# Optimization experiments

Hardware: AMD Instinct MI355X
Metric: run time of the kernel (lower is better)

The kernel has to match this reference:

```python
import jax, jax.numpy as jnp
import numpy as np

B, NPG, DEG = 8, 4096, 8          # graphs, nodes/graph, avg degree
N, E = B * NPG, B * NPG * DEG      # total nodes / directed edges
IN_C, HID, NCLS = 1024, 512, 4
K1, K2 = NPG // 2, NPG // 4        # ceil(0.5*NPG), ceil(0.5*K1)
NEG = 1e30                         # large-negative for masked scores


def setup_inputs() -> dict:
    key = jax.random.key(0)
    ks = jax.random.split(key, 20)
    gid = jnp.arange(E, dtype=jnp.int32) // (NPG * DEG)  # graph id per edge
    edge_src = jax.random.randint(ks[0], (E,), 0, NPG, dtype=jnp.int32) + gid * NPG
    edge_dst = jax.random.randint(ks[1], (E,), 0, NPG, dtype=jnp.int32) + gid * NPG
    x = jax.random.normal(ks[2], (N, IN_C), jnp.float32)

    def w(k, shape):
        fan_in = shape[0]
        return jax.random.normal(k, shape, jnp.float32) * (1.0 / np.sqrt(fan_in))

    return dict(
        x=x, edge_src=edge_src, edge_dst=edge_dst,
        W1=w(ks[3], (IN_C, HID)), b1=jnp.zeros((HID,), jnp.float32),
        p1_wr=w(ks[4], (HID, 1)), p1_br=jnp.zeros((1,), jnp.float32), p1_wo=w(ks[5], (HID, 1)),
        W2=w(ks[6], (HID, HID)), b2=jnp.zeros((HID,), jnp.float32),
        p2_wr=w(ks[7], (HID, 1)), p2_br=jnp.zeros((1,), jnp.float32), p2_wo=w(ks[8], (HID, 1)),
        W3=w(ks[9], (HID, HID)), b3=jnp.zeros((HID,), jnp.float32),
        fc1_w=w(ks[10], (2 * HID, HID)), fc1_b=jnp.zeros((HID,), jnp.float32),
        fc2_w=w(ks[11], (HID, NCLS)), fc2_b=jnp.zeros((NCLS,), jnp.float32),
    )


def _gcn(x, src, dst, emask, nmask, W, b):
    # PyG GCNConv: add self-loops, sym-normalize, aggregate, bias.
    h = x @ W                                             # [N,H]
    deg = jax.ops.segment_sum(emask, dst, num_segments=N) + nmask  # self-loop for active nodes
    dinv = jnp.where(deg > 0, jax.lax.rsqrt(deg), 0.0)
    coef = dinv[src] * dinv[dst] * emask                  # [E]
    out = jax.ops.segment_sum(h[src] * coef[:, None], dst, num_segments=N)
    out = out + (dinv * dinv * nmask)[:, None] * h + b    # self-loop term + bias
    return out


def _sag_pool(x, src, dst, emask, nmask, wr, br, wo, k):
    # PyG SAGPooling(GraphConv score, ratio): keep per-graph top-k, x *= tanh(score).
    agg = jax.ops.segment_sum(x[src] * emask[:, None], dst, num_segments=N)
    score = (agg @ wr + br + x @ wo)[:, 0]                # GraphConv(HID->1)
    score = jnp.where(nmask > 0, score, -NEG)
    order = jnp.argsort(-score.reshape(B, NPG), axis=1)
    ranks = jnp.argsort(order, axis=1)                    # rank within graph, descending score
    keep = (ranks < k).reshape(-1).astype(x.dtype) * nmask
    x2 = x * jnp.tanh(score)[:, None] * keep[:, None]
    emask2 = emask * keep[src] * keep[dst]                # filter edges to kept nodes
    return x2, emask2, keep


def reference(x, edge_src, edge_dst,
              W1, b1, p1_wr, p1_br, p1_wo,
              W2, b2, p2_wr, p2_br, p2_wo,
              W3, b3, fc1_w, fc1_b, fc2_w, fc2_b):
    src, dst = edge_src, edge_dst
    lrelu = lambda t: jax.nn.leaky_relu(t, 0.01)
    nmask = jnp.ones((N,), x.dtype)
    emask = jnp.ones((E,), x.dtype)

    h = lrelu(_gcn(x, src, dst, emask, nmask, W1, b1))
    h, emask, nmask = _sag_pool(h, src, dst, emask, nmask, p1_wr, p1_br, p1_wo, K1)
    h = lrelu(_gcn(h, src, dst, emask, nmask, W2, b2))
    h, emask, nmask = _sag_pool(h, src, dst, emask, nmask, p2_wr, p2_br, p2_wo, K2)
    h = lrelu(_gcn(h, src, dst, emask, nmask, W3, b3))

    hb = h.reshape(B, NPG, HID)
    mb = nmask.reshape(B, NPG)
    x_mean = (hb * mb[..., None]).sum(1) / mb.sum(1)[:, None]   # global_mean_pool over kept nodes
    x_max = jnp.where(mb[..., None] > 0, hb, -jnp.inf).max(1)   # global_max_pool
    g = jnp.concatenate([x_mean, x_max], axis=1)                # [B, 2H]; dropout is eval-mode identity
    g = lrelu(g @ fc1_w + fc1_b)
    return g @ fc2_w + fc2_b                                    # [B, NCLS]
```

## Files before the change

### kernel.cpp

```cpp
#include <hip/hip_runtime.h>

#define N_NODES 32768
#define NPG_    4096
#define NB_     8
#define E_EDGES 262144
#define IN_C_   1024
#define HID_    512
#define NOUT_   512
#define K1_     2048
#define K2_     1024

typedef _Float16 half4_t __attribute__((ext_vector_type(4)));
typedef _Float16 half8_t __attribute__((ext_vector_type(8)));
typedef float    floatx4 __attribute__((ext_vector_type(4)));

__device__ __forceinline__ float lrelu(float v) { return v > 0.f ? v : 0.01f * v; }

template <bool AFP32>
__global__ __launch_bounds__(256) void gemm_split_kernel(
    const float* __restrict__ A32,
    const _Float16* __restrict__ Ah, const _Float16* __restrict__ Al,
    const _Float16* __restrict__ Bh, const _Float16* __restrict__ Bl,
    float* __restrict__ C, int K) {
  __shared__ __align__(16) _Float16 sAh[128][64];
  __shared__ __align__(16) _Float16 sAl[128][64];
  __shared__ __align__(16) _Float16 sBh[128][64];
  __shared__ __align__(16) _Float16 sBl[128][64];

  const int t    = threadIdx.x;
  const int bm   = blockIdx.y * 128;
  const int bn   = blockIdx.x * 128;
  const int lane = t & 63;
  const int wv   = t >> 6;
  const int wr   = wv >> 1;
  const int wc   = wv & 1;
  const int fr   = lane & 15;
  const int kg   = lane >> 4;

  floatx4 zero = {0.f, 0.f, 0.f, 0.f};
  floatx4 acc[4][4];
#pragma unroll
  for (int i = 0; i < 4; ++i)
#pragma unroll
    for (int j = 0; j < 4; ++j) acc[i][j] = zero;

  for (int kt = 0; kt < K; kt += 64) {
#pragma unroll
    for (int l = 0; l < 4; ++l) {
      const int idx = l * 256 + t;
      const int row = idx >> 3;
      const int slot = idx & 7;
      const int col = ((slot ^ (row & 7)) << 3);
      *(half8_t*)&sBh[row][col] = *(const half8_t*)(Bh + (size_t)(bn + row) * K + kt + slot * 8);
      *(half8_t*)&sBl[row][col] = *(const half8_t*)(Bl + (size_t)(bn + row) * K + kt + slot * 8);
    }
    if constexpr (AFP32) {
#pragma unroll
      for (int l = 0; l < 8; ++l) {
        const int idx = l * 256 + t;
        const int row = idx >> 4;
        const int c4  = idx & 15;
        const float4 v = *(const float4*)(A32 + (size_t)(bm + row) * K + kt + c4 * 4);
        const _Float16 h0 = (_Float16)v.x, h1 = (_Float16)v.y,
                       h2 = (_Float16)v.z, h3 = (_Float16)v.w;
        half4_t hh = {h0, h1, h2, h3};
        half4_t hl = {(_Float16)(v.x - (float)h0), (_Float16)(v.y - (float)h1),
                      (_Float16)(v.z - (float)h2), (_Float16)(v.w - (float)h3)};
        const int slot = c4 >> 1;
        const int col  = ((slot ^ (row & 7)) << 3) + (c4 & 1) * 4;
        *(half4_t*)&sAh[row][col] = hh;
        *(half4_t*)&sAl[row][col] = hl;
      }
    } else {
#pragma unroll
      for (int l = 0; l < 4; ++l) {
        const int idx = l * 256 + t;
        const int row = idx >> 3;
        const int slot = idx & 7;
        const int col = ((slot ^ (row & 7)) << 3);
        *(half8_t*)&sAh[row][col] = *(const half8_t*)(Ah + (size_t)(bm + row) * K + kt + slot * 8);
        *(half8_t*)&sAl[row][col] = *(const half8_t*)(Al + (size_t)(bm + row) * K + kt + slot * 8);
      }
    }
    __syncthreads();

#pragma unroll
    for (int ks = 0; ks < 2; ++ks) {
      half8_t ahf[4], alf[4], bhf[4], blf[4];
      const int slot = ks * 4 + kg;
#pragma unroll
      for (int i = 0; i < 4; ++i) {
        const int row = wr * 64 + i * 16 + fr;
        const int col = ((slot ^ (row & 7)) << 3);
        ahf[i] = *(const half8_t*)&sAh[row][col];
        alf[i] = *(const half8_t*)&sAl[row][col];
      }
#pragma unroll
      for (int j = 0; j < 4; ++j) {
        const int nrow = wc * 64 + j * 16 + fr;
        const int col  = ((slot ^ (nrow & 7)) << 3);
        bhf[j] = *(const half8_t*)&sBh[nrow][col];
        blf[j] = *(const half8_t*)&sBl[nrow][col];
      }
#pragma unroll
      for (int i = 0; i < 4; ++i)
#pragma unroll
        for (int j = 0; j < 4; ++j) {
          acc[i][j] = __builtin_amdgcn_mfma_f32_16x16x32_f16(ahf[i], bhf[j], acc[i][j], 0, 0, 0);
          acc[i][j] = __builtin_amdgcn_mfma_f32_16x16x32_f16(ahf[i], blf[j], acc[i][j], 0, 0, 0);
          acc[i][j] = __builtin_amdgcn_mfma_f32_16x16x32_f16(alf[i], bhf[j], acc[i][j], 0, 0, 0);
        }
    }
    __syncthreads();
  }

#pragma unroll
  for (int i = 0; i < 4; ++i)
#pragma unroll
    for (int j = 0; j < 4; ++j) {
      const int row0 = bm + wr * 64 + i * 16 + kg * 4;
      const int col  = bn + wc * 64 + j * 16 + fr;
#pragma unroll
      for (int r = 0; r < 4; ++r)
        C[(size_t)(row0 + r) * NOUT_ + col] = acc[i][j][r];
    }
}

__global__ void split_w_kernel(const float* __restrict__ W, int K, int total,
                               _Float16* __restrict__ Wht, _Float16* __restrict__ Wlt) {
  const int idx = blockIdx.x * blockDim.x + threadIdx.x;
  if (idx >= total) return;
  const int n = idx / K;
  const int k = idx - n * K;
  const float v = W[(size_t)k * NOUT_ + n];
  const _Float16 h = (_Float16)v;
  Wht[idx] = h;
  Wlt[idx] = (_Float16)(v - (float)h);
}

__global__ void csr_count_kernel(const int* __restrict__ dst, int* __restrict__ cnt) {
  const int e = blockIdx.x * blockDim.x + threadIdx.x;
  if (e < E_EDGES) atomicAdd(&cnt[dst[e]], 1);
}

__global__ __launch_bounds__(1024) void exscan_kernel(const int* __restrict__ cnt,
                                                      int* __restrict__ ofs,
                                                      int* __restrict__ cur) {
  __shared__ int part[1024];
  const int t = threadIdx.x;
  const int base = t * 32;
  int loc[32];
  int s = 0;
#pragma unroll
  for (int i = 0; i < 32; ++i) { loc[i] = cnt[base + i]; s += loc[i]; }
  part[t] = s;
  __syncthreads();
  for (int off = 1; off < 1024; off <<= 1) {
    const int v = (t >= off) ? part[t - off] : 0;
    __syncthreads();
    part[t] += v;
    __syncthreads();
  }
  int run = (t > 0) ? part[t - 1] : 0;
#pragma unroll
  for (int i = 0; i < 32; ++i) { ofs[base + i] = run; cur[base + i] = run; run += loc[i]; }
  if (t == 1023) ofs[N_NODES] = run;
}

__global__ void csr_fill_kernel(const int* __restrict__ src, const int* __restrict__ dst,
                                int* __restrict__ cur, int* __restrict__ csr_src) {
  const int e = blockIdx.x * blockDim.x + threadIdx.x;
  if (e < E_EDGES) {
    const int p = atomicAdd(&cur[dst[e]], 1);
    csr_src[p] = src[e];
  }
}

__global__ void dinv_kernel(const int* __restrict__ ofs, const int* __restrict__ csr,
                            const float* __restrict__ m, float* __restrict__ dinv) {
  const int n = blockIdx.x * blockDim.x + threadIdx.x;
  if (n >= N_NODES) return;
  const float mn = m[n];
  float d = mn;
  if (mn > 0.f) {
    const int s = ofs[n], e = ofs[n + 1];
    for (int i = s; i < e; ++i) d += m[csr[i]];
  }
  dinv[n] = d > 0.f ? 1.f / sqrtf(d) : 0.f;
}

__global__ __launch_bounds__(128) void gcn_agg_kernel(const float* __restrict__ h,
                                                      const int* __restrict__ ofs,
                                                      const int* __restrict__ csr,
                                                      const float* __restrict__ dinv,
                                                      const float* __restrict__ bias,
                                                      float* __restrict__ out) {
  const int n = blockIdx.x;
  const int t = threadIdx.x;
  const float dn = dinv[n];
  float4 acc = {0.f, 0.f, 0.f, 0.f};
  if (dn > 0.f) {
    const int s = ofs[n], e = ofs[n + 1];
    for (int i = s; i < e; ++i) {
      const int sv = csr[i];
      const float c = dinv[sv] * dn;
      if (c != 0.f) {
        const float4 hv = *(const float4*)(h + (size_t)sv * HID_ + t * 4);
        acc.x += c * hv.x; acc.y += c * hv.y; acc.z += c * hv.z; acc.w += c * hv.w;
      }
    }
  }
  const float4 hv = *(const float4*)(h + (size_t)n * HID_ + t * 4);
  const float4 bv = *(const float4*)(bias + t * 4);
  const float sc = dn * dn;
  float4 r;
  r.x = lrelu(acc.x + sc * hv.x + bv.x);
  r.y = lrelu(acc.y + sc * hv.y + bv.y);
  r.z = lrelu(acc.z + sc * hv.z + bv.z);
  r.w = lrelu(acc.w + sc * hv.w + bv.w);
  *(float4*)(out + (size_t)n * HID_ + t * 4) = r;
}

__global__ __launch_bounds__(64) void node_dots_kernel(const float* __restrict__ h,
                                                       const float* __restrict__ wr,
                                                       const float* __restrict__ wo,
                                                       float* __restrict__ sr,
                                                       float* __restrict__ so) {
  const int n = blockIdx.x;
  const int t = threadIdx.x;
  const float4 h0 = *(const float4*)(h + (size_t)n * HID_ + t * 8);
  const float4 h1 = *(const float4*)(h + (size_t)n * HID_ + t * 8 + 4);
  const float4 r0 = *(const float4*)(wr + t * 8);
  const float4 r1 = *(const float4*)(wr + t * 8 + 4);
  const float4 o0 = *(const float4*)(wo + t * 8);
  const float4 o1 = *(const float4*)(wo + t * 8 + 4);
  float pr = h0.x * r0.x + h0.y * r0.y + h0.z * r0.z + h0.w * r0.w +
             h1.x * r1.x + h1.y * r1.y + h1.z * r1.z + h1.w * r1.w;
  float po = h0.x * o0.x + h0.y * o0.y + h0.z * o0.z + h0.w * o0.w +
             h1.x * o1.x + h1.y * o1.y + h1.z * o1.z + h1.w * o1.w;
#pragma unroll
  for (int off = 32; off; off >>= 1) {
    pr += __shfl_down(pr, off);
    po += __shfl_down(po, off);
  }
  if (t == 0) { sr[n] = pr; so[n] = po; }
}

__global__ void score_kernel(const int* __restrict__ ofs, const int* __restrict__ csr,
                             const float* __restrict__ sr, const float* __restrict__ so,
                             const float* __restrict__ m, const float* __restrict__ br,
                             float* __restrict__ score) {
  const int n = blockIdx.x * blockDim.x + threadIdx.x;
  if (n >= N_NODES) return;
  if (m[n] <= 0.f) { score[n] = -1e30f; return; }
  float s = 0.f;
  const int st = ofs[n], e = ofs[n + 1];
  for (int i = st; i < e; ++i) { const int sv = csr[i]; s += sr[sv] * m[sv]; }
  score[n] = s + so[n] + br[0];
}

__global__ __launch_bounds__(256) void topk_kernel(const float* __restrict__ score,
                                                   const float* __restrict__ m,
                                                   float* __restrict__ mout, int k) {
  __shared__ float ssc[NPG_];
  const int g   = blockIdx.x >> 4;
  const int blk = blockIdx.x & 15;
  const float* gs = score + g * NPG_;
  for (int i = threadIdx.x; i < NPG_; i += 256) ssc[i] = gs[i];
  __syncthreads();
  const int li = blk * 256 + threadIdx.x;
  const float mysc = ssc[li];
  int cnt = 0;
#pragma unroll 4
  for (int j = 0; j < NPG_; ++j) {
    const float sj = ssc[j];
    cnt += (sj > mysc) || (sj == mysc && j < li);
  }
  const int n = g * NPG_ + li;
  mout[n] = (cnt < k && m[n] > 0.f) ? 1.f : 0.f;
}

__global__ void pool_apply_split_kernel(const float* __restrict__ xin,
                                        const float* __restrict__ score,
                                        const float* __restrict__ keep,
                                        _Float16* __restrict__ Ph,
                                        _Float16* __restrict__ Pl) {
  const int i = blockIdx.x * blockDim.x + threadIdx.x;
  const int n = i >> 7;
  const float f = keep[n] > 0.f ? tanhf(score[n]) : 0.f;
  const float4 v = *(const float4*)(xin + (size_t)i * 4);
  const float x0 = v.x * f, x1 = v.y * f, x2 = v.z * f, x3 = v.w * f;
  const _Float16 h0 = (_Float16)x0, h1 = (_Float16)x1,
                 h2 = (_Float16)x2, h3 = (_Float16)x3;
  half4_t hh = {h0, h1, h2, h3};
  half4_t hl = {(_Float16)(x0 - (float)h0), (_Float16)(x1 - (float)h1),
                (_Float16)(x2 - (float)h2), (_Float16)(x3 - (float)h3)};
  *(half4_t*)(Ph + (size_t)i * 4) = hh;
  *(half4_t*)(Pl + (size_t)i * 4) = hl;
}

__global__ __launch_bounds__(512) void gpool1_kernel(const float* __restrict__ h,
                                                     const float* __restrict__ m,
                                                     float* __restrict__ psum,
                                                     float* __restrict__ pmax,
                                                     float* __restrict__ pcnt) {
  const int b = blockIdx.y;
  const int c = blockIdx.x;
  const int ch = threadIdx.x;
  const int base = b * NPG_ + c * 128;
  float s = 0.f, mx = -INFINITY, cv = 0.f;
  for (int i = 0; i < 128; ++i) {
    const float mv = m[base + i];
    const float hv = h[(size_t)(base + i) * HID_ + ch];
    s += mv * hv;
    if (mv > 0.f) mx = fmaxf(mx, hv);
    cv += mv;
  }
  const int p = b * 32 + c;
  psum[(size_t)p * HID_ + ch] = s;
  pmax[(size_t)p * HID_ + ch] = mx;
  if (ch == 0) pcnt[p] = cv;
}

__global__ __launch_bounds__(512) void gpool2_kernel(const float* __restrict__ psum,
                                                     const float* __restrict__ pmax,
                                                     const float* __restrict__ pcnt,
                                                     float* __restrict__ g) {
  const int b = blockIdx.x;
  const int ch = threadIdx.x;
  float s = 0.f, mx = -INFINITY, cv = 0.f;
  for (int c = 0; c < 32; ++c) {
    const int p = b * 32 + c;
    s += psum[(size_t)p * HID_ + ch];
    mx = fmaxf(mx, pmax[(size_t)p * HID_ + ch]);
    cv += pcnt[p];
  }
  g[b * 1024 + ch] = s / cv;
  g[b * 1024 + 512 + ch] = mx;
}

__global__ __launch_bounds__(64) void fc1_kernel(const float* __restrict__ g,
                                                 const float* __restrict__ w1,
                                                 const float* __restrict__ b1,
                                                 float* __restrict__ hbuf) {
  const int b = blockIdx.x;
  const int j = blockIdx.y * 64 + threadIdx.x;
  __shared__ float gs[2 * HID_];
  for (int i = threadIdx.x; i < 2 * HID_; i += 64) gs[i] = g[b * 1024 + i];
  __syncthreads();
  float s = b1[j];
#pragma unroll 4
  for (int i = 0; i < 2 * HID_; ++i) s += gs[i] * w1[i * HID_ + j];
  hbuf[b * HID_ + j] = lrelu(s);
}

__global__ __launch_bounds__(64) void fc2_kernel(const float* __restrict__ hbuf,
                                                 const float* __restrict__ w2,
                                                 const float* __restrict__ b2,
                                                 float* __restrict__ out) {
  const int b = blockIdx.x;
  const int t = threadIdx.x;
  float s0 = 0.f, s1 = 0.f, s2 = 0.f, s3 = 0.f;
  for (int i = t; i < HID_; i += 64) {
    const float hv = hbuf[b * HID_ + i];
    s0 += hv * w2[i * 4 + 0];
    s1 += hv * w2[i * 4 + 1];
    s2 += hv * w2[i * 4 + 2];
    s3 += hv * w2[i * 4 + 3];
  }
#pragma unroll
  for (int off = 32; off; off >>= 1) {
    s0 += __shfl_down(s0, off); s1 += __shfl_down(s1, off);
    s2 += __shfl_down(s2, off); s3 += __shfl_down(s3, off);
  }
  if (t == 0) {
    out[b * 4 + 0] = s0 + b2[0];
    out[b * 4 + 1] = s1 + b2[1];
    out[b * 4 + 2] = s2 + b2[2];
    out[b * 4 + 3] = s3 + b2[3];
  }
}

__global__ void set_ones_kernel(float* __restrict__ p, int n) {
  const int i = blockIdx.x * blockDim.x + threadIdx.x;
  if (i < n) p[i] = 1.f;
}

extern "C" void kernel_launch(void* const* d_in, const int* in_sizes, int n_in,
                              void* d_out, int out_size, void* d_ws, size_t ws_size,
                              hipStream_t stream) {
  const float* x        = (const float*)d_in[0];
  const int*   edge_src = (const int*)d_in[1];
  const int*   edge_dst = (const int*)d_in[2];
  const float* W1 = (const float*)d_in[3];
  const float* b1 = (const float*)d_in[4];
  const float* p1_wr = (const float*)d_in[5];
  const float* p1_br = (const float*)d_in[6];
  const float* p1_wo = (const float*)d_in[7];
  const float* W2 = (const float*)d_in[8];
  const float* b2 = (const float*)d_in[9];
  const float* p2_wr = (const float*)d_in[10];
  const float* p2_br = (const float*)d_in[11];
  const float* p2_wo = (const float*)d_in[12];
  const float* W3 = (const float*)d_in[13];
  const float* b3 = (const float*)d_in[14];
  const float* fc1_w = (const float*)d_in[15];
  const float* fc1_b = (const float*)d_in[16];
  const float* fc2_w = (const float*)d_in[17];
  const float* fc2_b = (const float*)d_in[18];
  float* out = (float*)d_out;

  size_t o = 0;
  auto alloc = [&](size_t bytes) {
    void* p = (char*)d_ws + o;
    o += (bytes + 255) & ~(size_t)255;
    return p;
  };
  float* R0 = (float*)alloc((size_t)N_NODES * HID_ * 4);
  float* R1 = (float*)alloc((size_t)N_NODES * HID_ * 4);
  _Float16* W1ht = (_Float16*)alloc((size_t)NOUT_ * IN_C_ * 2);
  _Float16* W1lt = (_Float16*)alloc((size_t)NOUT_ * IN_C_ * 2);
  _Float16* W2ht = (_Float16*)alloc((size_t)NOUT_ * HID_ * 2);
  _Float16* W2lt = (_Float16*)alloc((size_t)NOUT_ * HID_ * 2);
  _Float16* W3ht = (_Float16*)alloc((size_t)NOUT_ * HID_ * 2);
  _Float16* W3lt = (_Float16*)alloc((size_t)NOUT_ * HID_ * 2);
  int*   csr   = (int*)alloc((size_t)E_EDGES * 4);
  int*   ofs   = (int*)alloc((size_t)(N_NODES + 1) * 4);
  int*   cur   = (int*)alloc((size_t)N_NODES * 4);
  int*   cnt   = (int*)alloc((size_t)N_NODES * 4);
  float* dinvB = (float*)alloc((size_t)N_NODES * 4);
  float* mA    = (float*)alloc((size_t)N_NODES * 4);
  float* mB    = (float*)alloc((size_t)N_NODES * 4);
  float* srB   = (float*)alloc((size_t)N_NODES * 4);
  float* soB   = (float*)alloc((size_t)N_NODES * 4);
  float* scB   = (float*)alloc((size_t)N_NODES * 4);
  float* psum  = (float*)alloc((size_t)NB_ * 32 * HID_ * 4);
  float* pmax  = (float*)alloc((size_t)NB_ * 32 * HID_ * 4);
  float* pcnt  = (float*)alloc((size_t)NB_ * 32 * 4);
  float* gbuf  = (float*)alloc((size_t)NB_ * 1024 * 4);
  float* hbuf  = (float*)alloc((size_t)NB_ * HID_ * 4);

  _Float16* P1h = (_Float16*)R0;
  _Float16* P1l = P1h + (size_t)N_NODES * HID_;
  _Float16* P2h = (_Float16*)R1;
  _Float16* P2l = P2h + (size_t)N_NODES * HID_;

  hipMemsetAsync(cnt, 0, (size_t)N_NODES * 4, stream);
  csr_count_kernel<<<E_EDGES / 256, 256, 0, stream>>>(edge_dst, cnt);
  exscan_kernel<<<1, 1024, 0, stream>>>(cnt, ofs, cur);
  csr_fill_kernel<<<E_EDGES / 256, 256, 0, stream>>>(edge_src, edge_dst, cur, csr);
  set_ones_kernel<<<N_NODES / 256, 256, 0, stream>>>(mA, N_NODES);
  split_w_kernel<<<(NOUT_ * IN_C_) / 256, 256, 0, stream>>>(W1, IN_C_, NOUT_ * IN_C_, W1ht, W1lt);
  split_w_kernel<<<(NOUT_ * HID_) / 256, 256, 0, stream>>>(W2, HID_, NOUT_ * HID_, W2ht, W2lt);
  split_w_kernel<<<(NOUT_ * HID_) / 256, 256, 0, stream>>>(W3, HID_, NOUT_ * HID_, W3ht, W3lt);

  const dim3 gemm_grid(NOUT_ / 128, N_NODES / 128);

  gemm_split_kernel<true><<<gemm_grid, 256, 0, stream>>>(x, nullptr, nullptr,
                                                         W1ht, W1lt, R0, IN_C_);
  dinv_kernel<<<N_NODES / 256, 256, 0, stream>>>(ofs, csr, mA, dinvB);
  gcn_agg_kernel<<<N_NODES, 128, 0, stream>>>(R0, ofs, csr, dinvB, b1, R1);
  node_dots_kernel<<<N_NODES, 64, 0, stream>>>(R1, p1_wr, p1_wo, srB, soB);
  score_kernel<<<N_NODES / 256, 256, 0, stream>>>(ofs, csr, srB, soB, mA, p1_br, scB);
  topk_kernel<<<NB_ * 16, 256, 0, stream>>>(scB, mA, mB, K1_);
  pool_apply_split_kernel<<<(N_NODES * HID_ / 4) / 256, 256, 0, stream>>>(R1, scB, mB, P1h, P1l);

  gemm_split_kernel<false><<<gemm_grid, 256, 0, stream>>>(nullptr, P1h, P1l,
                                                          W2ht, W2lt, R1, HID_);
  dinv_kernel<<<N_NODES / 256, 256, 0, stream>>>(ofs, csr, mB, dinvB);
  gcn_agg_kernel<<<N_NODES, 128, 0, stream>>>(R1, ofs, csr, dinvB, b2, R0);
  node_dots_kernel<<<N_NODES, 64, 0, stream>>>(R0, p2_wr, p2_wo, srB, soB);
  score_kernel<<<N_NODES / 256, 256, 0, stream>>>(ofs, csr, srB, soB, mB, p2_br, scB);
  topk_kernel<<<NB_ * 16, 256, 0, stream>>>(scB, mB, mA, K2_);
  pool_apply_split_kernel<<<(N_NODES * HID_ / 4) / 256, 256, 0, stream>>>(R0, scB, mA, P2h, P2l);

  gemm_split_kernel<false><<<gemm_grid, 256, 0, stream>>>(nullptr, P2h, P2l,
                                                          W3ht, W3lt, R0, HID_);
  dinv_kernel<<<N_NODES / 256, 256, 0, stream>>>(ofs, csr, mA, dinvB);
  gcn_agg_kernel<<<N_NODES, 128, 0, stream>>>(R0, ofs, csr, dinvB, b3, R1);

  gpool1_kernel<<<dim3(32, NB_), 512, 0, stream>>>(R1, mA, psum, pmax, pcnt);
  gpool2_kernel<<<NB_, 512, 0, stream>>>(psum, pmax, pcnt, gbuf);
  fc1_kernel<<<dim3(NB_, HID_ / 64), 64, 0, stream>>>(gbuf, fc1_w, fc1_b, hbuf);
  fc2_kernel<<<NB_, 64, 0, stream>>>(hbuf, fc2_w, fc2_b, out);
}
```

Baseline: 1.009 ms.

## Fold source dinv scaling into GEMM epilogue and fuse score dots into aggregation

```diff
diff --git a/kernel.cpp b/kernel.cpp
--- a/kernel.cpp
+++ b/kernel.cpp
@@ -21,6 +21,7 @@
     const float* __restrict__ A32,
     const _Float16* __restrict__ Ah, const _Float16* __restrict__ Al,
     const _Float16* __restrict__ Bh, const _Float16* __restrict__ Bl,
+    const float* __restrict__ dinv,
     float* __restrict__ C, int K) {
   __shared__ __align__(16) _Float16 sAh[128][64];
   __shared__ __align__(16) _Float16 sAl[128][64];
@@ -28,8 +29,11 @@
   __shared__ __align__(16) _Float16 sBl[128][64];
 
   const int t    = threadIdx.x;
-  const int bm   = blockIdx.y * 128;
-  const int bn   = blockIdx.x * 128;
+  const int nwg  = gridDim.x;
+  const int per  = nwg >> 3;
+  const int id   = (blockIdx.x & 7) * per + (blockIdx.x >> 3);
+  const int bn   = (id & 3) * 128;
+  const int bm   = (id >> 2) * 128;
   const int lane = t & 63;
   const int wv   = t >> 6;
   const int wr   = wv >> 1;
@@ -115,15 +119,19 @@
   }
 
 #pragma unroll
-  for (int i = 0; i < 4; ++i)
+  for (int i = 0; i < 4; ++i) {
+    const int row0 = bm + wr * 64 + i * 16 + kg * 4;
+    float ds[4];
+#pragma unroll
+    for (int r = 0; r < 4; ++r) ds[r] = dinv[row0 + r];
 #pragma unroll
     for (int j = 0; j < 4; ++j) {
-      const int row0 = bm + wr * 64 + i * 16 + kg * 4;
-      const int col  = bn + wc * 64 + j * 16 + fr;
+      const int col = bn + wc * 64 + j * 16 + fr;
 #pragma unroll
       for (int r = 0; r < 4; ++r)
-        C[(size_t)(row0 + r) * NOUT_ + col] = acc[i][j][r];
-    }
+        C[(size_t)(row0 + r) * NOUT_ + col] = acc[i][j][r] * ds[r];
+    }
+  }
 }
 
 __global__ void split_w_kernel(const float* __restrict__ W, int K, int total,
@@ -189,61 +197,67 @@
   dinv[n] = d > 0.f ? 1.f / sqrtf(d) : 0.f;
 }
 
-__global__ __launch_bounds__(128) void gcn_agg_kernel(const float* __restrict__ h,
-                                                      const int* __restrict__ ofs,
-                                                      const int* __restrict__ csr,
-                                                      const float* __restrict__ dinv,
-                                                      const float* __restrict__ bias,
-                                                      float* __restrict__ out) {
-  const int n = blockIdx.x;
-  const int t = threadIdx.x;
+template <bool DOTS>
+__global__ __launch_bounds__(256) void gcn_agg_fused_kernel(
+    const float* __restrict__ hs,
+    const int* __restrict__ ofs, const int* __restrict__ csr,
+    const float* __restrict__ dinv, const float* __restrict__ bias,
+    const float* __restrict__ wr, const float* __restrict__ wo,
+    float* __restrict__ out, float* __restrict__ sr, float* __restrict__ so) {
+  const int n = blockIdx.x * 4 + (threadIdx.x >> 6);
+  const int t = threadIdx.x & 63;
+  const size_t c0 = (size_t)t * 8;
   const float dn = dinv[n];
-  float4 acc = {0.f, 0.f, 0.f, 0.f};
+  floatx4 a0 = {0.f, 0.f, 0.f, 0.f}, a1 = a0, b0 = a0, b1 = a0;
   if (dn > 0.f) {
     const int s = ofs[n], e = ofs[n + 1];
-    for (int i = s; i < e; ++i) {
-      const int sv = csr[i];
-      const float c = dinv[sv] * dn;
-      if (c != 0.f) {
-        const float4 hv = *(const float4*)(h + (size_t)sv * HID_ + t * 4);
-        acc.x += c * hv.x; acc.y += c * hv.y; acc.z += c * hv.z; acc.w += c * hv.w;
-      }
-    }
-  }
-  const float4 hv = *(const float4*)(h + (size_t)n * HID_ + t * 4);
-  const float4 bv = *(const float4*)(bias + t * 4);
-  const float sc = dn * dn;
-  float4 r;
-  r.x = lrelu(acc.x + sc * hv.x + bv.x);
-  r.y = lrelu(acc.y + sc * hv.y + bv.y);
-  r.z = lrelu(acc.z + sc * hv.z + bv.z);
-  r.w = lrelu(acc.w + sc * hv.w + bv.w);
-  *(float4*)(out + (size_t)n * HID_ + t * 4) = r;
-}
-
-__global__ __launch_bounds__(64) void node_dots_kernel(const float* __restrict__ h,
-                                                       const float* __restrict__ wr,
-                                                       const float* __restrict__ wo,
-                                                       float* __restrict__ sr,
-                                                       float* __restrict__ so) {
-  const int n = blockIdx.x;
-  const int t = threadIdx.x;
-  const float4 h0 = *(const float4*)(h + (size_t)n * HID_ + t * 8);
-  const float4 h1 = *(const float4*)(h + (size_t)n * HID_ + t * 8 + 4);
-  const float4 r0 = *(const float4*)(wr + t * 8);
-  const float4 r1 = *(const float4*)(wr + t * 8 + 4);
-  const float4 o0 = *(const float4*)(wo + t * 8);
-  const float4 o1 = *(const float4*)(wo + t * 8 + 4);
-  float pr = h0.x * r0.x + h0.y * r0.y + h0.z * r0.z + h0.w * r0.w +
-             h1.x * r1.x + h1.y * r1.y + h1.z * r1.z + h1.w * r1.w;
-  float po = h0.x * o0.x + h0.y * o0.y + h0.z * o0.z + h0.w * o0.w +
-             h1.x * o1.x + h1.y * o1.y + h1.z * o1.z + h1.w * o1.w;
-#pragma unroll
-  for (int off = 32; off; off >>= 1) {
-    pr += __shfl_down(pr, off);
-    po += __shfl_down(po, off);
-  }
-  if (t == 0) { sr[n] = pr; so[n] = po; }
+    int i = s;
+    for (; i + 2 <= e; i += 2) {
+      const int s0 = csr[i], s1 = csr[i + 1];
+      const floatx4 v00 = *(const floatx4*)(hs + (size_t)s0 * HID_ + c0);
+      const floatx4 v01 = *(const floatx4*)(hs + (size_t)s0 * HID_ + c0 + 4);
+      const floatx4 v10 = *(const floatx4*)(hs + (size_t)s1 * HID_ + c0);
+      const floatx4 v11 = *(const floatx4*)(hs + (size_t)s1 * HID_ + c0 + 4);
+      a0 += v00; a1 += v01; b0 += v10; b1 += v11;
+    }
+    if (i < e) {
+      const int s0 = csr[i];
+      a0 += *(const floatx4*)(hs + (size_t)s0 * HID_ + c0);
+      a1 += *(const floatx4*)(hs + (size_t)s0 * HID_ + c0 + 4);
+    }
+    a0 += *(const floatx4*)(hs + (size_t)n * HID_ + c0);
+    a1 += *(const floatx4*)(hs + (size_t)n * HID_ + c0 + 4);
+    a0 += b0; a1 += b1;
+  }
+  const floatx4 bv0 = *(const floatx4*)(bias + c0);
+  const floatx4 bv1 = *(const floatx4*)(bias + c0 + 4);
+  floatx4 r0, r1;
+#pragma unroll
+  for (int q = 0; q < 4; ++q) {
+    r0[q] = lrelu(dn * a0[q] + bv0[q]);
+    r1[q] = lrelu(dn * a1[q] + bv1[q]);
+  }
+  *(floatx4*)(out + (size_t)n * HID_ + c0)     = r0;
+  *(floatx4*)(out + (size_t)n * HID_ + c0 + 4) = r1;
+
+  if constexpr (DOTS) {
+    const floatx4 wr0 = *(const floatx4*)(wr + c0);
+    const floatx4 wr1 = *(const floatx4*)(wr + c0 + 4);
+    const floatx4 wo0 = *(const floatx4*)(wo + c0);
+    const floatx4 wo1 = *(const floatx4*)(wo + c0 + 4);
+    float pr = 0.f, po = 0.f;
+#pragma unroll
+    for (int q = 0; q < 4; ++q) {
+      pr += r0[q] * wr0[q] + r1[q] * wr1[q];
+      po += r0[q] * wo0[q] + r1[q] * wo1[q];
+    }
+#pragma unroll
+    for (int off = 32; off; off >>= 1) {
+      pr += __shfl_down(pr, off);
+      po += __shfl_down(po, off);
+    }
+    if (t == 0) { sr[n] = pr; so[n] = po; }
+  }
 }
 
 __global__ void score_kernel(const int* __restrict__ ofs, const int* __restrict__ csr,
@@ -454,30 +468,32 @@
   split_w_kernel<<<(NOUT_ * HID_) / 256, 256, 0, stream>>>(W2, HID_, NOUT_ * HID_, W2ht, W2lt);
   split_w_kernel<<<(NOUT_ * HID_) / 256, 256, 0, stream>>>(W3, HID_, NOUT_ * HID_, W3ht, W3lt);
 
-  const dim3 gemm_grid(NOUT_ / 128, N_NODES / 128);
-
+  const int gemm_grid = (NOUT_ / 128) * (N_NODES / 128);
+  const int agg_grid = N_NODES / 4;
+
+  dinv_kernel<<<N_NODES / 256, 256, 0, stream>>>(ofs, csr, mA, dinvB);
   gemm_split_kernel<true><<<gemm_grid, 256, 0, stream>>>(x, nullptr, nullptr,
-                                                         W1ht, W1lt, R0, IN_C_);
-  dinv_kernel<<<N_NODES / 256, 256, 0, stream>>>(ofs, csr, mA, dinvB);
-  gcn_agg_kernel<<<N_NODES, 128, 0, stream>>>(R0, ofs, csr, dinvB, b1, R1);
-  node_dots_kernel<<<N_NODES, 64, 0, stream>>>(R1, p1_wr, p1_wo, srB, soB);
+                                                         W1ht, W1lt, dinvB, R0, IN_C_);
+  gcn_agg_fused_kernel<true><<<agg_grid, 256, 0, stream>>>(R0, ofs, csr, dinvB, b1,
+                                                           p1_wr, p1_wo, R1, srB, soB);
   score_kernel<<<N_NODES / 256, 256, 0, stream>>>(ofs, csr, srB, soB, mA, p1_br, scB);
   topk_kernel<<<NB_ * 16, 256, 0, stream>>>(scB, mA, mB, K1_);
   pool_apply_split_kernel<<<(N_NODES * HID_ / 4) / 256, 256, 0, stream>>>(R1, scB, mB, P1h, P1l);
 
+  dinv_kernel<<<N_NODES / 256, 256, 0, stream>>>(ofs, csr, mB, dinvB);
   gemm_split_kernel<false><<<gemm_grid, 256, 0, stream>>>(nullptr, P1h, P1l,
-                                                          W2ht, W2lt, R1, HID_);
-  dinv_kernel<<<N_NODES / 256, 256, 0, stream>>>(ofs, csr, mB, dinvB);
-  gcn_agg_kernel<<<N_NODES, 128, 0, stream>>>(R1, ofs, csr, dinvB, b2, R0);
-  node_dots_kernel<<<N_NODES, 64, 0, stream>>>(R0, p2_wr, p2_wo, srB, soB);
+                                                          W2ht, W2lt, dinvB, R1, HID_);
+  gcn_agg_fused_kernel<true><<<agg_grid, 256, 0, stream>>>(R1, ofs, csr, dinvB, b2,
+                                                           p2_wr, p2_wo, R0, srB, soB);
   score_kernel<<<N_NODES / 256, 256, 0, stream>>>(ofs, csr, srB, soB, mB, p2_br, scB);
   topk_kernel<<<NB_ * 16, 256, 0, stream>>>(scB, mB, mA, K2_);
   pool_apply_split_kernel<<<(N_NODES * HID_ / 4) / 256, 256, 0, stream>>>(R0, scB, mA, P2h, P2l);
 
+  dinv_kernel<<<N_NODES / 256, 256, 0, stream>>>(ofs, csr, mA, dinvB);
   gemm_split_kernel<false><<<gemm_grid, 256, 0, stream>>>(nullptr, P2h, P2l,
-                                                          W3ht, W3lt, R0, HID_);
-  dinv_kernel<<<N_NODES / 256, 256, 0, stream>>>(ofs, csr, mA, dinvB);
-  gcn_agg_kernel<<<N_NODES, 128, 0, stream>>>(R0, ofs, csr, dinvB, b3, R1);
+                                                          W3ht, W3lt, dinvB, R0, HID_);
+  gcn_agg_fused_kernel<false><<<agg_grid, 256, 0, stream>>>(R0, ofs, csr, dinvB, b3,
+                                                            nullptr, nullptr, R1, nullptr, nullptr);
 
   gpool1_kernel<<<dim3(32, NB_), 512, 0, stream>>>(R1, mA, psum, pmax, pcnt);
   gpool2_kernel<<<NB_, 512, 0, stream>>>(psum, pmax, pcnt, gbuf);
```

Result: no change. 993.6 us (-1.5%).

## Prescale GEMM rows by dinv and aggregate per-graph channel slices in LDS

Applied to the files above, without the earlier changes.

```diff
diff --git a/kernel.cpp b/kernel.cpp
--- a/kernel.cpp
+++ b/kernel.cpp
@@ -21,6 +21,7 @@
     const float* __restrict__ A32,
     const _Float16* __restrict__ Ah, const _Float16* __restrict__ Al,
     const _Float16* __restrict__ Bh, const _Float16* __restrict__ Bl,
+    const float* __restrict__ dinv,
     float* __restrict__ C, int K) {
   __shared__ __align__(16) _Float16 sAh[128][64];
   __shared__ __align__(16) _Float16 sAl[128][64];
@@ -28,8 +29,11 @@
   __shared__ __align__(16) _Float16 sBl[128][64];
 
   const int t    = threadIdx.x;
-  const int bm   = blockIdx.y * 128;
-  const int bn   = blockIdx.x * 128;
+  const int nwg  = gridDim.x;
+  const int per  = nwg >> 3;
+  const int id   = (blockIdx.x & 7) * per + (blockIdx.x >> 3);
+  const int bn   = (id & 3) * 128;
+  const int bm   = (id >> 2) * 128;
   const int lane = t & 63;
   const int wv   = t >> 6;
   const int wr   = wv >> 1;
@@ -115,15 +119,19 @@
   }
 
 #pragma unroll
-  for (int i = 0; i < 4; ++i)
+  for (int i = 0; i < 4; ++i) {
+    const int row0 = bm + wr * 64 + i * 16 + kg * 4;
+    float ds[4];
+#pragma unroll
+    for (int r = 0; r < 4; ++r) ds[r] = dinv[row0 + r];
 #pragma unroll
     for (int j = 0; j < 4; ++j) {
-      const int row0 = bm + wr * 64 + i * 16 + kg * 4;
-      const int col  = bn + wc * 64 + j * 16 + fr;
+      const int col = bn + wc * 64 + j * 16 + fr;
 #pragma unroll
       for (int r = 0; r < 4; ++r)
-        C[(size_t)(row0 + r) * NOUT_ + col] = acc[i][j][r];
+        C[(size_t)(row0 + r) * NOUT_ + col] = acc[i][j][r] * ds[r];
     }
+  }
 }
 
 __global__ void split_w_kernel(const float* __restrict__ W, int K, int total,
@@ -189,36 +197,50 @@
   dinv[n] = d > 0.f ? 1.f / sqrtf(d) : 0.f;
 }
 
-__global__ __launch_bounds__(128) void gcn_agg_kernel(const float* __restrict__ h,
-                                                      const int* __restrict__ ofs,
-                                                      const int* __restrict__ csr,
-                                                      const float* __restrict__ dinv,
-                                                      const float* __restrict__ bias,
-                                                      float* __restrict__ out) {
-  const int n = blockIdx.x;
-  const int t = threadIdx.x;
-  const float dn = dinv[n];
-  float4 acc = {0.f, 0.f, 0.f, 0.f};
-  if (dn > 0.f) {
-    const int s = ofs[n], e = ofs[n + 1];
-    for (int i = s; i < e; ++i) {
-      const int sv = csr[i];
-      const float c = dinv[sv] * dn;
-      if (c != 0.f) {
-        const float4 hv = *(const float4*)(h + (size_t)sv * HID_ + t * 4);
-        acc.x += c * hv.x; acc.y += c * hv.y; acc.z += c * hv.z; acc.w += c * hv.w;
+__global__ __launch_bounds__(256) void gcn_agg_slice_kernel(
+    const float* __restrict__ hs,
+    const int* __restrict__ ofs, const int* __restrict__ csr,
+    const float* __restrict__ dinv, const float* __restrict__ bias,
+    float* __restrict__ out) {
+  __shared__ float slab[NPG_ * 4];
+  const int g    = blockIdx.x & 7;
+  const int c0   = (blockIdx.x >> 3) * 4;
+  const int t    = threadIdx.x;
+  const int base = g * NPG_;
+
+#pragma unroll
+  for (int r = 0; r < 16; ++r) {
+    const int n = r * 256 + t;
+    *(floatx4*)&slab[n * 4] = *(const floatx4*)(hs + (size_t)(base + n) * HID_ + c0);
+  }
+  __syncthreads();
+
+  const int ch = t & 3;
+  const int dl = t >> 2;
+  const float bv = bias[c0 + ch];
+  for (int chunk = 0; chunk < NPG_ / 64; ++chunk) {
+    const int dst = chunk * 64 + dl;
+    const int nn  = base + dst;
+    const float dn = dinv[nn];
+    float r;
+    if (dn > 0.f) {
+      float acc = slab[dst * 4 + ch];
+      float a2  = 0.f;
+      const int s = ofs[nn], e = ofs[nn + 1];
+      int i = s;
+      for (; i + 2 <= e; i += 2) {
+        const int s0 = csr[i] - base, s1 = csr[i + 1] - base;
+        acc += slab[s0 * 4 + ch];
+        a2  += slab[s1 * 4 + ch];
       }
+      if (i < e) acc += slab[(csr[i] - base) * 4 + ch];
+      acc += a2;
+      r = lrelu(dn * acc + bv);
+    } else {
+      r = lrelu(bv);
     }
-  }
-  const float4 hv = *(const float4*)(h + (size_t)n * HID_ + t * 4);
-  const float4 bv = *(const float4*)(bias + t * 4);
-  const float sc = dn * dn;
-  float4 r;
-  r.x = lrelu(acc.x + sc * hv.x + bv.x);
-  r.y = lrelu(acc.y + sc * hv.y + bv.y);
-  r.z = lrelu(acc.z + sc * hv.z + bv.z);
-  r.w = lrelu(acc.w + sc * hv.w + bv.w);
-  *(float4*)(out + (size_t)n * HID_ + t * 4) = r;
+    out[(size_t)nn * HID_ + c0 + ch] = r;
+  }
 }
 
 __global__ __launch_bounds__(64) void node_dots_kernel(const float* __restrict__ h,
@@ -454,30 +476,31 @@
   split_w_kernel<<<(NOUT_ * HID_) / 256, 256, 0, stream>>>(W2, HID_, NOUT_ * HID_, W2ht, W2lt);
   split_w_kernel<<<(NOUT_ * HID_) / 256, 256, 0, stream>>>(W3, HID_, NOUT_ * HID_, W3ht, W3lt);
 
-  const dim3 gemm_grid(NOUT_ / 128, N_NODES / 128);
-
+  const int gemm_grid = (NOUT_ / 128) * (N_NODES / 128);
+  const int agg_grid  = NB_ * (HID_ / 4);
+
+  dinv_kernel<<<N_NODES / 256, 256, 0, stream>>>(ofs, csr, mA, dinvB);
   gemm_split_kernel<true><<<gemm_grid, 256, 0, stream>>>(x, nullptr, nullptr,
-                                                         W1ht, W1lt, R0, IN_C_);
-  dinv_kernel<<<N_NODES / 256, 256, 0, stream>>>(ofs, csr, mA, dinvB);
-  gcn_agg_kernel<<<N_NODES, 128, 0, stream>>>(R0, ofs, csr, dinvB, b1, R1);
+                                                         W1ht, W1lt, dinvB, R0, IN_C_);
+  gcn_agg_slice_kernel<<<agg_grid, 256, 0, stream>>>(R0, ofs, csr, dinvB, b1, R1);
   node_dots_kernel<<<N_NODES, 64, 0, stream>>>(R1, p1_wr, p1_wo, srB, soB);
   score_kernel<<<N_NODES / 256, 256, 0, stream>>>(ofs, csr, srB, soB, mA, p1_br, scB);
   topk_kernel<<<NB_ * 16, 256, 0, stream>>>(scB, mA, mB, K1_);
   pool_apply_split_kernel<<<(N_NODES * HID_ / 4) / 256, 256, 0, stream>>>(R1, scB, mB, P1h, P1l);
 
+  dinv_kernel<<<N_NODES / 256, 256, 0, stream>>>(ofs, csr, mB, dinvB);
   gemm_split_kernel<false><<<gemm_grid, 256, 0, stream>>>(nullptr, P1h, P1l,
-                                                          W2ht, W2lt, R1, HID_);
-  dinv_kernel<<<N_NODES / 256, 256, 0, stream>>>(ofs, csr, mB, dinvB);
-  gcn_agg_kernel<<<N_NODES, 128, 0, stream>>>(R1, ofs, csr, dinvB, b2, R0);
+                                                          W2ht, W2lt, dinvB, R1, HID_);
+  gcn_agg_slice_kernel<<<agg_grid, 256, 0, stream>>>(R1, ofs, csr, dinvB, b2, R0);
   node_dots_kernel<<<N_NODES, 64, 0, stream>>>(R0, p2_wr, p2_wo, srB, soB);
   score_kernel<<<N_NODES / 256, 256, 0, stream>>>(ofs, csr, srB, soB, mB, p2_br, scB);
   topk_kernel<<<NB_ * 16, 256, 0, stream>>>(scB, mB, mA, K2_);
   pool_apply_split_kernel<<<(N_NODES * HID_ / 4) / 256, 256, 0, stream>>>(R0, scB, mA, P2h, P2l);
 
+  dinv_kernel<<<N_NODES / 256, 256, 0, stream>>>(ofs, csr, mA, dinvB);
   gemm_split_kernel<false><<<gemm_grid, 256, 0, stream>>>(nullptr, P2h, P2l,
-                                                          W3ht, W3lt, R0, HID_);
-  dinv_kernel<<<N_NODES / 256, 256, 0, stream>>>(ofs, csr, mA, dinvB);
-  gcn_agg_kernel<<<N_NODES, 128, 0, stream>>>(R0, ofs, csr, dinvB, b3, R1);
+                                                          W3ht, W3lt, dinvB, R0, HID_);
+  gcn_agg_slice_kernel<<<agg_grid, 256, 0, stream>>>(R0, ofs, csr, dinvB, b3, R1);
 
   gpool1_kernel<<<dim3(32, NB_), 512, 0, stream>>>(R1, mA, psum, pmax, pcnt);
   gpool2_kernel<<<NB_, 512, 0, stream>>>(psum, pmax, pcnt, gbuf);
```

New measurement: 1.475 ms. 46.2% more time.
